# Performance work log

Hardware: AMD Instinct MI355X
Metric: run time of the kernel (lower is better)

The kernel has to match this reference:

```python
import jax, jax.numpy as jnp
import numpy as np

N_NODES = 100000
N_EDGES = 1600000
STATE_DIM = 128
HID = 32


def _glorot(key, shape):
    fan_in, fan_out = shape
    lim = jnp.sqrt(6.0 / (fan_in + fan_out))
    return jax.random.uniform(key, shape, jnp.float32, -lim, lim)


def setup_inputs() -> dict:
    key = jax.random.key(0)
    ks = jax.random.split(key, 10)
    x = jax.random.normal(ks[0], (N_NODES, STATE_DIM), jnp.float32)
    edge_index = jax.random.randint(ks[1], (2, N_EDGES), 0, N_NODES, jnp.int32)
    params = {
        "W1": _glorot(ks[2], (STATE_DIM, HID)), "b1": jnp.zeros((HID,), jnp.float32),
        "Wh": _glorot(ks[3], (HID, HID)),        "bh": jnp.zeros((HID,), jnp.float32),
        "W2": _glorot(ks[4], (HID, 1)),          "b2": jnp.zeros((1,), jnp.float32),
        "Ws": _glorot(ks[5], (HID, 1)),          "bs": jnp.zeros((1,), jnp.float32),
    }
    return {"x": x, "edge_index": edge_index, **params}


def _gcn_norm(edge_index, n):
    # PyG GCNConv: add self-loops, symmetric normalization D^-1/2 (A+I) D^-1/2
    src, dst = edge_index[0], edge_index[1]
    ones = jnp.ones((src.shape[0],), jnp.float32)
    deg = jax.ops.segment_sum(ones, dst, num_segments=n) + 1.0  # +1 for self-loop
    dinv = jax.lax.rsqrt(deg)  # deg >= 1, always finite
    edge_norm = dinv[src] * dinv[dst]          # [E]
    self_norm = dinv * dinv                    # [N]
    return edge_norm, self_norm


def _gcn_conv(h, W, b, src, dst, edge_norm, self_norm, n):
    # transform first (PyG order), then normalized aggregation
    h = h @ W                                                   # [N, out]
    msg = h[src] * edge_norm[:, None]                           # [E, out] gather
    agg = jax.ops.segment_sum(msg, dst, num_segments=n)         # scatter-add
    return agg + h * self_norm[:, None] + b


def reference(x, edge_index, W1, b1, Wh, bh, W2, b2, Ws, bs):
    n = x.shape[0]
    src, dst = edge_index[0], edge_index[1]
    edge_norm, self_norm = _gcn_norm(edge_index, n)
    h = _gcn_conv(x, W1, b1, src, dst, edge_norm, self_norm, n)
    h = _gcn_conv(h, Wh, bh, src, dst, edge_norm, self_norm, n)
    mu = jax.nn.relu(h)
    mu = _gcn_conv(mu, W2, b2, src, dst, edge_norm, self_norm, n)
    std = _gcn_conv(h, Ws, bs, src, dst, edge_norm, self_norm, n)
    return (mu, std)
```

## Files before the change

### kernel.cpp

```cpp
#include <hip/hip_runtime.h>

#define NN 100000
#define NE 1600000
#define SD 128
#define HD 32
#define NBK 391
#define EPB 4000
#define NBLK 400
#define MAXBE 6144

__global__ __launch_bounds__(256) void k_p1(const int* __restrict__ dst,
                                            unsigned* __restrict__ bktcnt,
                                            unsigned* __restrict__ blockbase) {
    __shared__ unsigned h[NBK];
    int blk = blockIdx.x, tid = threadIdx.x;
    for (int i = tid; i < NBK; i += 256) h[i] = 0;
    __syncthreads();
    int e0 = blk * EPB;
    for (int i = tid; i < EPB; i += 256)
        atomicAdd(&h[(unsigned)dst[e0 + i] >> 8], 1u);
    __syncthreads();
    for (int i = tid; i < NBK; i += 256)
        blockbase[blk * NBK + i] = atomicAdd(&bktcnt[i], h[i]);
}

__global__ __launch_bounds__(512) void k_p2(const unsigned* __restrict__ bktcnt,
                                            unsigned* __restrict__ bktbase,
                                            unsigned* __restrict__ rowptr) {
    __shared__ unsigned sc[512];
    int tid = threadIdx.x;
    unsigned c = (tid < NBK) ? bktcnt[tid] : 0u;
    sc[tid] = c;
    __syncthreads();
    for (int off = 1; off < 512; off <<= 1) {
        unsigned t = (tid >= off) ? sc[tid - off] : 0u;
        __syncthreads();
        sc[tid] += t;
        __syncthreads();
    }
    if (tid <= NBK) bktbase[tid] = sc[tid] - c;
    if (tid == 0) rowptr[NN] = NE;
}

__global__ __launch_bounds__(256) void k_p3(const int* __restrict__ src,
                                            const int* __restrict__ dst,
                                            const unsigned* __restrict__ bktbase,
                                            const unsigned* __restrict__ blockbase,
                                            unsigned* __restrict__ ebuf) {
    __shared__ unsigned cur[NBK];
    int blk = blockIdx.x, tid = threadIdx.x;
    for (int i = tid; i < NBK; i += 256)
        cur[i] = bktbase[i] + blockbase[blk * NBK + i];
    __syncthreads();
    int e0 = blk * EPB;
    for (int i = tid; i < EPB; i += 256) {
        int d = dst[e0 + i];
        unsigned s = (unsigned)src[e0 + i];
        unsigned b = (unsigned)d >> 8;
        unsigned pos = atomicAdd(&cur[b], 1u);
        ebuf[pos] = ((unsigned)(d & 255) << 20) | s;
    }
}

__global__ __launch_bounds__(256) void k_p4(unsigned* __restrict__ ebuf,
                                            const unsigned* __restrict__ bktbase,
                                            unsigned* __restrict__ rowptr,
                                            float* __restrict__ dinv) {
    __shared__ unsigned eL[MAXBE];
    __shared__ unsigned hist[256];
    __shared__ unsigned sc[256];
    int b = blockIdx.x, tid = threadIdx.x;
    unsigned base = bktbase[b], nE = bktbase[b + 1] - base;
    int n0 = b << 8;
    int nodes = min(256, NN - n0);
    for (unsigned i = tid; i < nE; i += 256) eL[i] = ebuf[base + i];
    hist[tid] = 0;
    __syncthreads();
    for (unsigned i = tid; i < nE; i += 256) atomicAdd(&hist[eL[i] >> 20], 1u);
    __syncthreads();
    unsigned c = hist[tid];
    sc[tid] = c;
    __syncthreads();
    for (int off = 1; off < 256; off <<= 1) {
        unsigned t = (tid >= off) ? sc[tid - off] : 0u;
        __syncthreads();
        sc[tid] += t;
        __syncthreads();
    }
    unsigned excl = sc[tid] - c;
    if (tid < nodes) {
        rowptr[n0 + tid] = base + excl;
        dinv[n0 + tid] = rsqrtf((float)c + 1.0f);
    }
    hist[tid] = base + excl;
    __syncthreads();
    for (unsigned i = tid; i < nE; i += 256) {
        unsigned v = eL[i];
        unsigned pos = atomicAdd(&hist[v >> 20], 1u);
        ebuf[pos] = v & 0xFFFFFu;
    }
}

__global__ __launch_bounds__(256) void k_mm128(const float* __restrict__ X,
                                               const float* __restrict__ W,
                                               const float* __restrict__ dinv,
                                               float* __restrict__ out) {
    __shared__ float Wls[SD * HD];
    __shared__ float xT[32][260];
    int tid = threadIdx.x;
    {
        const float4* W4 = (const float4*)W;
        float4* Wl4 = (float4*)Wls;
        for (int i = tid; i < SD * HD / 4; i += 256) Wl4[i] = W4[i];
    }
    int nb = blockIdx.x * 256;
    int g = tid & 7;
    int q = tid >> 3;
    float acc[8][4] = {};
    for (int kc = 0; kc < SD; kc += 32) {
        __syncthreads();
        for (int i = tid; i < 256 * 8; i += 256) {
            int n = i >> 3, k4 = i & 7;
            int node = nb + n;
            float4 v = (node < NN) ? *(const float4*)&X[(size_t)node * SD + kc + k4 * 4]
                                   : make_float4(0.f, 0.f, 0.f, 0.f);
            xT[k4 * 4 + 0][n] = v.x;
            xT[k4 * 4 + 1][n] = v.y;
            xT[k4 * 4 + 2][n] = v.z;
            xT[k4 * 4 + 3][n] = v.w;
        }
        __syncthreads();
#pragma unroll
        for (int kk = 0; kk < 32; ++kk) {
            const float4 xa = *(const float4*)&xT[kk][q * 8];
            const float4 xb = *(const float4*)&xT[kk][q * 8 + 4];
            const float4 wv = *(const float4*)&Wls[(kc + kk) * HD + g * 4];
            acc[0][0] = fmaf(xa.x, wv.x, acc[0][0]);
            acc[0][1] = fmaf(xa.x, wv.y, acc[0][1]);
            acc[0][2] = fmaf(xa.x, wv.z, acc[0][2]);
            acc[0][3] = fmaf(xa.x, wv.w, acc[0][3]);
            acc[1][0] = fmaf(xa.y, wv.x, acc[1][0]);
            acc[1][1] = fmaf(xa.y, wv.y, acc[1][1]);
            acc[1][2] = fmaf(xa.y, wv.z, acc[1][2]);
            acc[1][3] = fmaf(xa.y, wv.w, acc[1][3]);
            acc[2][0] = fmaf(xa.z, wv.x, acc[2][0]);
            acc[2][1] = fmaf(xa.z, wv.y, acc[2][1]);
            acc[2][2] = fmaf(xa.z, wv.z, acc[2][2]);
            acc[2][3] = fmaf(xa.z, wv.w, acc[2][3]);
            acc[3][0] = fmaf(xa.w, wv.x, acc[3][0]);
            acc[3][1] = fmaf(xa.w, wv.y, acc[3][1]);
            acc[3][2] = fmaf(xa.w, wv.z, acc[3][2]);
            acc[3][3] = fmaf(xa.w, wv.w, acc[3][3]);
            acc[4][0] = fmaf(xb.x, wv.x, acc[4][0]);
            acc[4][1] = fmaf(xb.x, wv.y, acc[4][1]);
            acc[4][2] = fmaf(xb.x, wv.z, acc[4][2]);
            acc[4][3] = fmaf(xb.x, wv.w, acc[4][3]);
            acc[5][0] = fmaf(xb.y, wv.x, acc[5][0]);
            acc[5][1] = fmaf(xb.y, wv.y, acc[5][1]);
            acc[5][2] = fmaf(xb.y, wv.z, acc[5][2]);
            acc[5][3] = fmaf(xb.y, wv.w, acc[5][3]);
            acc[6][0] = fmaf(xb.z, wv.x, acc[6][0]);
            acc[6][1] = fmaf(xb.z, wv.y, acc[6][1]);
            acc[6][2] = fmaf(xb.z, wv.z, acc[6][2]);
            acc[6][3] = fmaf(xb.z, wv.w, acc[6][3]);
            acc[7][0] = fmaf(xb.w, wv.x, acc[7][0]);
            acc[7][1] = fmaf(xb.w, wv.y, acc[7][1]);
            acc[7][2] = fmaf(xb.w, wv.z, acc[7][2]);
            acc[7][3] = fmaf(xb.w, wv.w, acc[7][3]);
        }
    }
#pragma unroll
    for (int r = 0; r < 8; ++r) {
        int node = nb + q * 8 + r;
        if (node < NN) {
            float dv = dinv[node];
            float4 o = {acc[r][0] * dv, acc[r][1] * dv, acc[r][2] * dv, acc[r][3] * dv};
            *(float4*)&out[(size_t)node * HD + g * 4] = o;
        }
    }
}

template <int MODE>
__global__ __launch_bounds__(256) void k_gather(const unsigned* __restrict__ edat,
                                                const unsigned* __restrict__ rowptr,
                                                const float* __restrict__ dinv,
                                                const float* __restrict__ hw,
                                                const float* __restrict__ bias,
                                                const float* __restrict__ Wa,
                                                const float* __restrict__ Wb,
                                                float* __restrict__ outw) {
    int gid = blockIdx.x * 256 + threadIdx.x;
    int n = gid >> 5, j = gid & 31;
    unsigned s0 = rowptr[n], s1 = rowptr[n + 1];
    float acc = 0.f;
    unsigned i = s0;
    for (; i + 4 <= s1; i += 4) {
        unsigned e0 = edat[i], e1 = edat[i + 1], e2 = edat[i + 2], e3 = edat[i + 3];
        float v0 = hw[(size_t)e0 * HD + j];
        float v1 = hw[(size_t)e1 * HD + j];
        float v2 = hw[(size_t)e2 * HD + j];
        float v3 = hw[(size_t)e3 * HD + j];
        acc += (v0 + v1) + (v2 + v3);
    }
    for (; i < s1; ++i) acc += hw[(size_t)edat[i] * HD + j];
    float dv = dinv[n];
    float v = dv * (acc + hw[(size_t)n * HD + j]) + bias[j];
    if (MODE == 1) {
        float h2 = 0.f;
#pragma unroll
        for (int jj = 0; jj < 32; ++jj)
            h2 = fmaf(__shfl(v, jj, 32), Wa[jj * HD + j], h2);
        outw[(size_t)n * HD + j] = h2 * dv;
    } else {
        float a = fmaxf(v, 0.f) * Wa[j];
        float b = v * Wb[j];
#pragma unroll
        for (int off = 16; off > 0; off >>= 1) {
            a += __shfl_xor(a, off, 32);
            b += __shfl_xor(b, off, 32);
        }
        if (j == 0) ((float2*)outw)[n] = make_float2(a * dv, b * dv);
    }
}

__global__ __launch_bounds__(256) void k_gscal(const unsigned* __restrict__ edat,
                                               const unsigned* __restrict__ rowptr,
                                               const float* __restrict__ dinv,
                                               const float2* __restrict__ head_w,
                                               const float* __restrict__ b2,
                                               const float* __restrict__ bs,
                                               float* __restrict__ out) {
    int gid = blockIdx.x * 256 + threadIdx.x;
    int n = gid >> 5, l = gid & 31;
    unsigned s0 = rowptr[n], s1 = rowptr[n + 1];
    float a = 0.f, b = 0.f;
    for (unsigned i = s0 + l; i < s1; i += 32) {
        float2 w = head_w[edat[i]];
        a += w.x; b += w.y;
    }
#pragma unroll
    for (int off = 16; off > 0; off >>= 1) {
        a += __shfl_xor(a, off, 32);
        b += __shfl_xor(b, off, 32);
    }
    if (l == 0) {
        float dv = dinv[n];
        float2 self = head_w[n];
        out[n]      = dv * (a + self.x) + b2[0];
        out[NN + n] = dv * (b + self.y) + bs[0];
    }
}

extern "C" void kernel_launch(void* const* d_in, const int* in_sizes, int n_in,
                              void* d_out, int out_size, void* d_ws, size_t ws_size,
                              hipStream_t stream) {
    const float* x   = (const float*)d_in[0];
    const int*   ei  = (const int*)d_in[1];
    const int*   src = ei;
    const int*   dst = ei + NE;
    const float* W1  = (const float*)d_in[2];
    const float* b1  = (const float*)d_in[3];
    const float* Wh  = (const float*)d_in[4];
    const float* bh  = (const float*)d_in[5];
    const float* W2  = (const float*)d_in[6];
    const float* b2  = (const float*)d_in[7];
    const float* Wsp = (const float*)d_in[8];
    const float* bs  = (const float*)d_in[9];
    float* out = (float*)d_out;

    unsigned* w         = (unsigned*)d_ws;
    unsigned* edat      = w;
    unsigned* blockbase = w + 1600000;
    float*    hw1       = (float*)(w + 1760000);
    float*    hw2       = (float*)(w + 4960000);
    unsigned* rowptr    = w + 8160000;
    unsigned* bktcnt    = w + 8260004;
    unsigned* bktbase   = w + 8260400;
    float*    dinv      = (float*)(w + 8260800);
    float*    headw     = (float*)(w + 8360800);

    hipMemsetAsync(bktcnt, 0, NBK * sizeof(unsigned), stream);
    k_p1<<<NBLK, 256, 0, stream>>>(dst, bktcnt, blockbase);
    k_p2<<<1, 512, 0, stream>>>(bktcnt, bktbase, rowptr);
    k_p3<<<NBLK, 256, 0, stream>>>(src, dst, bktbase, blockbase, edat);
    k_p4<<<NBK, 256, 0, stream>>>(edat, bktbase, rowptr, dinv);

    k_mm128<<<(NN + 255) / 256, 256, 0, stream>>>(x, W1, dinv, hw1);
    k_gather<1><<<NN * HD / 256, 256, 0, stream>>>(edat, rowptr, dinv, hw1, b1, Wh, nullptr, hw2);
    k_gather<2><<<NN * HD / 256, 256, 0, stream>>>(edat, rowptr, dinv, hw2, bh, W2, Wsp, headw);
    k_gscal<<<NN * HD / 256, 256, 0, stream>>>(edat, rowptr, dinv, (const float2*)headw, b2, bs, out);
}
```

Before: 286.4 us.

## Split hidden features into 8-wide channel slices for cache-friendly gathers

Stores the 32-wide hidden features as four 8-float channel slices so each gather pass over a slice touches a smaller working set (100K×8 floats) that fits in cache better. The gathers now process 8 edges in parallel per wavefront with 8 lanes per edge and reduce with shuffles. The second matmul and the head partial sums move into separate kernels (k_mmB, k_hsum). The edge list is now read once per channel instead of once overall, and two extra launches are added.

```diff
diff --git a/kernel.cpp b/kernel.cpp
--- a/kernel.cpp
+++ b/kernel.cpp
@@ -4,6 +4,8 @@
 #define NE 1600000
 #define SD 128
 #define HD 32
+#define NCH 4
+#define CW 8
 #define NBK 391
 #define EPB 4000
 #define NBLK 400
@@ -104,7 +106,7 @@
 __global__ __launch_bounds__(256) void k_mm128(const float* __restrict__ X,
                                                const float* __restrict__ W,
                                                const float* __restrict__ dinv,
-                                               float* __restrict__ out) {
+                                               float* __restrict__ hw1c) {
     __shared__ float Wls[SD * HD];
     __shared__ float xT[32][260];
     int tid = threadIdx.x;
@@ -169,57 +171,128 @@
             acc[7][3] = fmaf(xb.w, wv.w, acc[7][3]);
         }
     }
+    int c = g >> 1, jo = (g & 1) * 4;
 #pragma unroll
     for (int r = 0; r < 8; ++r) {
         int node = nb + q * 8 + r;
         if (node < NN) {
             float dv = dinv[node];
             float4 o = {acc[r][0] * dv, acc[r][1] * dv, acc[r][2] * dv, acc[r][3] * dv};
-            *(float4*)&out[(size_t)node * HD + g * 4] = o;
+            *(float4*)&hw1c[(size_t)c * NN * CW + (size_t)node * CW + jo] = o;
         }
     }
 }
 
-template <int MODE>
-__global__ __launch_bounds__(256) void k_gather(const unsigned* __restrict__ edat,
-                                                const unsigned* __restrict__ rowptr,
-                                                const float* __restrict__ dinv,
-                                                const float* __restrict__ hw,
-                                                const float* __restrict__ bias,
-                                                const float* __restrict__ Wa,
-                                                const float* __restrict__ Wb,
-                                                float* __restrict__ outw) {
-    int gid = blockIdx.x * 256 + threadIdx.x;
-    int n = gid >> 5, j = gid & 31;
+__global__ __launch_bounds__(256) void k_g1(const unsigned* __restrict__ edat,
+                                            const unsigned* __restrict__ rowptr,
+                                            const float* __restrict__ dinv,
+                                            const float* __restrict__ hwc,
+                                            const float* __restrict__ bias,
+                                            float* __restrict__ vbuf) {
+    int c = blockIdx.y;
+    const float* slice = hwc + (size_t)c * NN * CW;
+    int tid = threadIdx.x;
+    int n = blockIdx.x * 4 + (tid >> 6);
+    int lane = tid & 63;
+    int er = lane >> 3, j = lane & 7;
     unsigned s0 = rowptr[n], s1 = rowptr[n + 1];
     float acc = 0.f;
     unsigned i = s0;
-    for (; i + 4 <= s1; i += 4) {
-        unsigned e0 = edat[i], e1 = edat[i + 1], e2 = edat[i + 2], e3 = edat[i + 3];
-        float v0 = hw[(size_t)e0 * HD + j];
-        float v1 = hw[(size_t)e1 * HD + j];
-        float v2 = hw[(size_t)e2 * HD + j];
-        float v3 = hw[(size_t)e3 * HD + j];
-        acc += (v0 + v1) + (v2 + v3);
-    }
-    for (; i < s1; ++i) acc += hw[(size_t)edat[i] * HD + j];
+    for (; i + 16 <= s1; i += 16) {
+        unsigned ea = __builtin_nontemporal_load(&edat[i + er]);
+        unsigned eb = __builtin_nontemporal_load(&edat[i + 8 + er]);
+        float va = slice[(size_t)ea * CW + j];
+        float vb = slice[(size_t)eb * CW + j];
+        acc += va + vb;
+    }
+    if (i + 8 <= s1) {
+        acc += slice[(size_t)__builtin_nontemporal_load(&edat[i + er]) * CW + j];
+        i += 8;
+    }
+    if (i + er < s1)
+        acc += slice[(size_t)__builtin_nontemporal_load(&edat[i + er]) * CW + j];
+    acc += __shfl_xor(acc, 8);
+    acc += __shfl_xor(acc, 16);
+    acc += __shfl_xor(acc, 32);
     float dv = dinv[n];
-    float v = dv * (acc + hw[(size_t)n * HD + j]) + bias[j];
-    if (MODE == 1) {
-        float h2 = 0.f;
+    float v = dv * (acc + slice[(size_t)n * CW + j]) + bias[c * CW + j];
+    if (lane < CW)
+        __builtin_nontemporal_store(v, &vbuf[(size_t)c * NN * CW + (size_t)n * CW + j]);
+}
+
+__global__ __launch_bounds__(256) void k_mmB(const float* __restrict__ vbuf,
+                                             const float* __restrict__ Wh,
+                                             const float* __restrict__ dinv,
+                                             float* __restrict__ h2c) {
+    __shared__ float Wls[HD * HD];
+    int tid = threadIdx.x;
+    for (int i = tid; i < HD * HD; i += 256) Wls[i] = Wh[i];
+    __syncthreads();
+    int n = blockIdx.x * 8 + (tid >> 5);
+    int j = tid & 31;
+    float vj = vbuf[(size_t)(j >> 3) * NN * CW + (size_t)n * CW + (j & 7)];
+    float h2 = 0.f;
 #pragma unroll
-        for (int jj = 0; jj < 32; ++jj)
-            h2 = fmaf(__shfl(v, jj, 32), Wa[jj * HD + j], h2);
-        outw[(size_t)n * HD + j] = h2 * dv;
-    } else {
-        float a = fmaxf(v, 0.f) * Wa[j];
-        float b = v * Wb[j];
-#pragma unroll
-        for (int off = 16; off > 0; off >>= 1) {
-            a += __shfl_xor(a, off, 32);
-            b += __shfl_xor(b, off, 32);
-        }
-        if (j == 0) ((float2*)outw)[n] = make_float2(a * dv, b * dv);
+    for (int jj = 0; jj < 32; ++jj)
+        h2 = fmaf(__shfl(vj, jj, 32), Wls[jj * HD + j], h2);
+    h2c[(size_t)(j >> 3) * NN * CW + (size_t)n * CW + (j & 7)] = h2 * dinv[n];
+}
+
+__global__ __launch_bounds__(256) void k_g2(const unsigned* __restrict__ edat,
+                                            const unsigned* __restrict__ rowptr,
+                                            const float* __restrict__ dinv,
+                                            const float* __restrict__ h2c,
+                                            const float* __restrict__ bh,
+                                            const float* __restrict__ W2,
+                                            const float* __restrict__ Ws,
+                                            float2* __restrict__ hpart) {
+    int c = blockIdx.y;
+    const float* slice = h2c + (size_t)c * NN * CW;
+    int tid = threadIdx.x;
+    int n = blockIdx.x * 4 + (tid >> 6);
+    int lane = tid & 63;
+    int er = lane >> 3, j = lane & 7;
+    unsigned s0 = rowptr[n], s1 = rowptr[n + 1];
+    float acc = 0.f;
+    unsigned i = s0;
+    for (; i + 16 <= s1; i += 16) {
+        unsigned ea = __builtin_nontemporal_load(&edat[i + er]);
+        unsigned eb = __builtin_nontemporal_load(&edat[i + 8 + er]);
+        float va = slice[(size_t)ea * CW + j];
+        float vb = slice[(size_t)eb * CW + j];
+        acc += va + vb;
+    }
+    if (i + 8 <= s1) {
+        acc += slice[(size_t)__builtin_nontemporal_load(&edat[i + er]) * CW + j];
+        i += 8;
+    }
+    if (i + er < s1)
+        acc += slice[(size_t)__builtin_nontemporal_load(&edat[i + er]) * CW + j];
+    acc += __shfl_xor(acc, 8);
+    acc += __shfl_xor(acc, 16);
+    acc += __shfl_xor(acc, 32);
+    float dv = dinv[n];
+    float v2 = dv * (acc + slice[(size_t)n * CW + j]) + bh[c * CW + j];
+    float pa = fmaxf(v2, 0.f) * W2[c * CW + j];
+    float pb = v2 * Ws[c * CW + j];
+    pa += __shfl_xor(pa, 1); pb += __shfl_xor(pb, 1);
+    pa += __shfl_xor(pa, 2); pb += __shfl_xor(pb, 2);
+    pa += __shfl_xor(pa, 4); pb += __shfl_xor(pb, 4);
+    if (lane == 0) hpart[(size_t)c * NN + n] = make_float2(pa, pb);
+}
+
+__global__ __launch_bounds__(256) void k_hsum(const float2* __restrict__ hpart,
+                                              const float* __restrict__ dinv,
+                                              float2* __restrict__ headw) {
+    int n = blockIdx.x * 256 + threadIdx.x;
+    if (n < NN) {
+        float2 s0 = hpart[n];
+        float2 s1 = hpart[NN + n];
+        float2 s2 = hpart[2 * NN + n];
+        float2 s3 = hpart[3 * NN + n];
+        float dv = dinv[n];
+        headw[n] = make_float2(dv * ((s0.x + s1.x) + (s2.x + s3.x)),
+                               dv * ((s0.y + s1.y) + (s2.y + s3.y)));
     }
 }
 
@@ -270,14 +343,15 @@
 
     unsigned* w         = (unsigned*)d_ws;
     unsigned* edat      = w;
-    unsigned* blockbase = w + 1600000;
-    float*    hw1       = (float*)(w + 1760000);
-    float*    hw2       = (float*)(w + 4960000);
-    unsigned* rowptr    = w + 8160000;
-    unsigned* bktcnt    = w + 8260004;
-    unsigned* bktbase   = w + 8260400;
-    float*    dinv      = (float*)(w + 8260800);
-    float*    headw     = (float*)(w + 8360800);
+    float*    hw1c      = (float*)(w + 1600000);
+    float*    vbuf      = (float*)(w + 4800000);
+    unsigned* blockbase = w + 4800000;
+    float2*   hpart     = (float2*)(w + 4800000);
+    unsigned* rowptr    = w + 8000000;
+    unsigned* bktcnt    = w + 8100004;
+    unsigned* bktbase   = w + 8100400;
+    float*    dinv      = (float*)(w + 8100800);
+    float2*   headw     = (float2*)(w + 8200800);
 
     hipMemsetAsync(bktcnt, 0, NBK * sizeof(unsigned), stream);
     k_p1<<<NBLK, 256, 0, stream>>>(dst, bktcnt, blockbase);
@@ -285,8 +359,10 @@
     k_p3<<<NBLK, 256, 0, stream>>>(src, dst, bktbase, blockbase, edat);
     k_p4<<<NBK, 256, 0, stream>>>(edat, bktbase, rowptr, dinv);
 
-    k_mm128<<<(NN + 255) / 256, 256, 0, stream>>>(x, W1, dinv, hw1);
-    k_gather<1><<<NN * HD / 256, 256, 0, stream>>>(edat, rowptr, dinv, hw1, b1, Wh, nullptr, hw2);
-    k_gather<2><<<NN * HD / 256, 256, 0, stream>>>(edat, rowptr, dinv, hw2, bh, W2, Wsp, headw);
-    k_gscal<<<NN * HD / 256, 256, 0, stream>>>(edat, rowptr, dinv, (const float2*)headw, b2, bs, out);
-}
+    k_mm128<<<(NN + 255) / 256, 256, 0, stream>>>(x, W1, dinv, hw1c);
+    k_g1<<<dim3(NN / 4, NCH), 256, 0, stream>>>(edat, rowptr, dinv, hw1c, b1, vbuf);
+    k_mmB<<<NN / 8, 256, 0, stream>>>(vbuf, Wh, dinv, hw1c);
+    k_g2<<<dim3(NN / 4, NCH), 256, 0, stream>>>(edat, rowptr, dinv, hw1c, bh, W2, Wsp, hpart);
+    k_hsum<<<(NN + 255) / 256, 256, 0, stream>>>(hpart, dinv, headw);
+    k_gscal<<<NN * HD / 256, 256, 0, stream>>>(edat, rowptr, dinv, headw, b2, bs, out);
+}
```

Measured after the change: 502.7 us. 1.76x slower.

## Store hidden node features as packed bf16 and gather two edges per warp

Applied to the files above, without the earlier changes.

The intermediate 32-wide node feature tables are now stored as packed bf16 pairs (16 words per node) instead of fp32, which halves the bytes read per edge in the two gather kernels. Each 32-lane group now splits into two halves, each half handling a different edge, and the halves are combined with a shuffle. Wh is staged in shared memory for the per-node matmul. The cost is bf16 rounding error in the aggregated features, plus extra unpack and shuffle instructions.

```diff
diff --git a/kernel.cpp b/kernel.cpp
--- a/kernel.cpp
+++ b/kernel.cpp
@@ -4,10 +4,21 @@
 #define NE 1600000
 #define SD 128
 #define HD 32
+#define RW 16
 #define NBK 391
 #define EPB 4000
 #define NBLK 400
 #define MAXBE 6144
+
+static __device__ __forceinline__ unsigned bf16pk(float a, float b) {
+    unsigned ua = __float_as_uint(a);
+    ua = (ua + 0x7fffu + ((ua >> 16) & 1u)) >> 16;
+    unsigned ub = __float_as_uint(b);
+    ub = (ub + 0x7fffu + ((ub >> 16) & 1u)) >> 16;
+    return ua | (ub << 16);
+}
+static __device__ __forceinline__ float bflo(unsigned u) { return __uint_as_float(u << 16); }
+static __device__ __forceinline__ float bfhi(unsigned u) { return __uint_as_float(u & 0xffff0000u); }
 
 __global__ __launch_bounds__(256) void k_p1(const int* __restrict__ dst,
                                             unsigned* __restrict__ bktcnt,
@@ -104,7 +115,7 @@
 __global__ __launch_bounds__(256) void k_mm128(const float* __restrict__ X,
                                                const float* __restrict__ W,
                                                const float* __restrict__ dinv,
-                                               float* __restrict__ out) {
+                                               unsigned* __restrict__ hw1) {
     __shared__ float Wls[SD * HD];
     __shared__ float xT[32][260];
     int tid = threadIdx.x;
@@ -174,8 +185,9 @@
         int node = nb + q * 8 + r;
         if (node < NN) {
             float dv = dinv[node];
-            float4 o = {acc[r][0] * dv, acc[r][1] * dv, acc[r][2] * dv, acc[r][3] * dv};
-            *(float4*)&out[(size_t)node * HD + g * 4] = o;
+            uint2 pk = make_uint2(bf16pk(acc[r][0] * dv, acc[r][1] * dv),
+                                  bf16pk(acc[r][2] * dv, acc[r][3] * dv));
+            *(uint2*)&hw1[(size_t)node * RW + g * 2] = pk;
         }
     }
 }
@@ -184,42 +196,65 @@
 __global__ __launch_bounds__(256) void k_gather(const unsigned* __restrict__ edat,
                                                 const unsigned* __restrict__ rowptr,
                                                 const float* __restrict__ dinv,
-                                                const float* __restrict__ hw,
+                                                const unsigned* __restrict__ tbl,
                                                 const float* __restrict__ bias,
                                                 const float* __restrict__ Wa,
                                                 const float* __restrict__ Wb,
-                                                float* __restrict__ outw) {
-    int gid = blockIdx.x * 256 + threadIdx.x;
-    int n = gid >> 5, j = gid & 31;
+                                                unsigned* __restrict__ outt,
+                                                float2* __restrict__ headw) {
+    __shared__ float Wls[HD * HD];
+    int tid = threadIdx.x;
+    if (MODE == 1) {
+        for (int i = tid; i < HD * HD; i += 256) Wls[i] = Wa[i];
+        __syncthreads();
+    }
+    int n = blockIdx.x * 8 + (tid >> 5);
+    int l = tid & 31;
+    int e = l >> 4, p = l & 15;
     unsigned s0 = rowptr[n], s1 = rowptr[n + 1];
-    float acc = 0.f;
+    float acc0 = 0.f, acc1 = 0.f;
     unsigned i = s0;
     for (; i + 4 <= s1; i += 4) {
-        unsigned e0 = edat[i], e1 = edat[i + 1], e2 = edat[i + 2], e3 = edat[i + 3];
-        float v0 = hw[(size_t)e0 * HD + j];
-        float v1 = hw[(size_t)e1 * HD + j];
-        float v2 = hw[(size_t)e2 * HD + j];
-        float v3 = hw[(size_t)e3 * HD + j];
-        acc += (v0 + v1) + (v2 + v3);
-    }
-    for (; i < s1; ++i) acc += hw[(size_t)edat[i] * HD + j];
+        unsigned ea = edat[i + e], eb = edat[i + 2 + e];
+        unsigned ua = tbl[(size_t)ea * RW + p];
+        unsigned ub = tbl[(size_t)eb * RW + p];
+        acc0 += bflo(ua) + bflo(ub);
+        acc1 += bfhi(ua) + bfhi(ub);
+    }
+    if (i + 2 <= s1) {
+        unsigned ua = tbl[(size_t)edat[i + e] * RW + p];
+        acc0 += bflo(ua); acc1 += bfhi(ua);
+        i += 2;
+    }
+    if (i + e < s1) {
+        unsigned ua = tbl[(size_t)edat[i + e] * RW + p];
+        acc0 += bflo(ua); acc1 += bfhi(ua);
+    }
+    acc0 += __shfl_xor(acc0, 16);
+    acc1 += __shfl_xor(acc1, 16);
     float dv = dinv[n];
-    float v = dv * (acc + hw[(size_t)n * HD + j]) + bias[j];
+    unsigned su = tbl[(size_t)n * RW + p];
+    float v0 = dv * (acc0 + bflo(su)) + bias[2 * p];
+    float v1 = dv * (acc1 + bfhi(su)) + bias[2 * p + 1];
     if (MODE == 1) {
-        float h2 = 0.f;
-#pragma unroll
-        for (int jj = 0; jj < 32; ++jj)
-            h2 = fmaf(__shfl(v, jj, 32), Wa[jj * HD + j], h2);
-        outw[(size_t)n * HD + j] = h2 * dv;
+        float o0 = 0.f, o1 = 0.f;
+#pragma unroll
+        for (int q = 0; q < 16; ++q) {
+            float sv0 = __shfl(v0, q, 16);
+            float sv1 = __shfl(v1, q, 16);
+            o0 += sv0 * Wls[(2 * q) * HD + 2 * p] + sv1 * Wls[(2 * q + 1) * HD + 2 * p];
+            o1 += sv0 * Wls[(2 * q) * HD + 2 * p + 1] + sv1 * Wls[(2 * q + 1) * HD + 2 * p + 1];
+        }
+        if (l < 16) outt[(size_t)n * RW + p] = bf16pk(o0 * dv, o1 * dv);
     } else {
-        float a = fmaxf(v, 0.f) * Wa[j];
-        float b = v * Wb[j];
-#pragma unroll
-        for (int off = 16; off > 0; off >>= 1) {
-            a += __shfl_xor(a, off, 32);
-            b += __shfl_xor(b, off, 32);
-        }
-        if (j == 0) ((float2*)outw)[n] = make_float2(a * dv, b * dv);
+        float pa = fmaxf(v0, 0.f) * Wa[2 * p] + fmaxf(v1, 0.f) * Wa[2 * p + 1];
+        float pb = v0 * Wb[2 * p] + v1 * Wb[2 * p + 1];
+#pragma unroll
+        for (int off = 8; off > 0; off >>= 1) {
+            pa += __shfl_xor(pa, off);
+            pb += __shfl_xor(pb, off);
+        }
+        if (l == 0) headw[n] = make_float2(pa * dv, pb * dv);
     }
 }
 
@@ -270,14 +305,14 @@
 
     unsigned* w         = (unsigned*)d_ws;
     unsigned* edat      = w;
-    unsigned* blockbase = w + 1600000;
-    float*    hw1       = (float*)(w + 1760000);
-    float*    hw2       = (float*)(w + 4960000);
-    unsigned* rowptr    = w + 8160000;
-    unsigned* bktcnt    = w + 8260004;
-    unsigned* bktbase   = w + 8260400;
-    float*    dinv      = (float*)(w + 8260800);
-    float*    headw     = (float*)(w + 8360800);
+    unsigned* hw1       = w + 1600000;
+    unsigned* hw2       = w + 3200000;
+    unsigned* blockbase = w + 4800000;
+    unsigned* rowptr    = w + 5000000;
+    unsigned* bktcnt    = w + 5100004;
+    unsigned* bktbase   = w + 5100500;
+    float*    dinv      = (float*)(w + 5101000);
+    float2*   headw     = (float2*)(w + 5201000);
 
     hipMemsetAsync(bktcnt, 0, NBK * sizeof(unsigned), stream);
     k_p1<<<NBLK, 256, 0, stream>>>(dst, bktcnt, blockbase);
@@ -286,7 +321,7 @@
     k_p4<<<NBK, 256, 0, stream>>>(edat, bktbase, rowptr, dinv);
 
     k_mm128<<<(NN + 255) / 256, 256, 0, stream>>>(x, W1, dinv, hw1);
-    k_gather<1><<<NN * HD / 256, 256, 0, stream>>>(edat, rowptr, dinv, hw1, b1, Wh, nullptr, hw2);
-    k_gather<2><<<NN * HD / 256, 256, 0, stream>>>(edat, rowptr, dinv, hw2, bh, W2, Wsp, headw);
-    k_gscal<<<NN * HD / 256, 256, 0, stream>>>(edat, rowptr, dinv, (const float2*)headw, b2, bs, out);
-}
+    k_gather<1><<<NN / 8, 256, 0, stream>>>(edat, rowptr, dinv, hw1, b1, Wh, nullptr, hw2, nullptr);
+    k_gather<2><<<NN / 8, 256, 0, stream>>>(edat, rowptr, dinv, hw2, bh, W2, Wsp, nullptr, headw);
+    k_gscal<<<NN * HD / 256, 256, 0, stream>>>(edat, rowptr, dinv, headw, b2, bs, out);
+}
```

After: 302.7 us. +5.7%, slower.
